# Optimization experiments

Measured on AMD Instinct MI355X. Metric: run time of the kernel, lower is better.

Reference implementation:

```python
import jax, jax.numpy as jnp
import numpy as np

B, V_IN, V_OUT, C_IN, C_OUT, SPIRAL, K_NNZ = 4, 12500, 50000, 64, 32, 9, 3

def setup_inputs() -> dict:
    key = jax.random.key(0)
    k1, k2, k3, k4, k5 = jax.random.split(key, 5)
    x = jax.random.normal(k1, (B, V_IN, C_IN), dtype=jnp.float32)
    spiral_indices = jax.random.randint(k2, (V_OUT, SPIRAL), 0, V_OUT)
    up_idx = jax.random.randint(k3, (V_OUT, K_NNZ), 0, V_IN)
    up_val = jax.random.uniform(k4, (V_OUT, K_NNZ), dtype=jnp.float32)
    weight = jax.random.normal(k5, (SPIRAL * C_IN, C_OUT), dtype=jnp.float32) / np.sqrt(SPIRAL * C_IN)
    bias = jnp.zeros((C_OUT,), dtype=jnp.float32)
    return {"x": x, "spiral_indices": spiral_indices, "up_idx": up_idx,
            "up_val": up_val, "weight": weight, "bias": bias}

def reference(x, spiral_indices, up_idx, up_val, weight, bias):
    # pool_bvc: sparse up_transform @ x, 3 nnz per output vertex
    # x: [B, V_in, C]; up_idx/up_val: [V_out, K]
    up = jnp.einsum('bvkc,vk->bvc', x[:, up_idx], up_val)  # [B, V_out, C_in]
    # SpiralConv: gather spiral neighborhoods, flatten, linear
    g = up[:, spiral_indices]                               # [B, V_out, S, C_in]
    g = g.reshape(g.shape[0], g.shape[1], -1)               # [B, V_out, S*C_in]
    y = jnp.einsum('bvf,fo->bvo', g, weight) + bias         # [B, V_out, C_out]
    return jax.nn.relu(y)
```

## Files before the change

### kernel.cpp

```cpp
#include <hip/hip_runtime.h>
#include <hip/hip_bf16.h>

#define B_     4
#define V_IN   12500
#define V_OUT  50000
#define C_IN   64
#define C_OUT  32
#define SPIRAL 9
#define K_NNZ  3
#define ROWS   (B_ * V_OUT)
#define KDIM   (SPIRAL * C_IN)
#define KSTEPS (KDIM / 32)
#define WFRAG_ELEMS (KSTEPS * 2 * 64 * 8)

#define GROUPS_PER_B (V_OUT / 16)
#define G1           2048
#define TILES_PER_B  782
#define G2           1024

typedef __attribute__((ext_vector_type(8))) short short8_t;
typedef __attribute__((ext_vector_type(4))) float floatx4;

__device__ __forceinline__ unsigned short f32_to_bf16(float f) {
    unsigned int u = __float_as_uint(f);
    unsigned int r = u + 0x7fffu + ((u >> 16) & 1u);
    return (unsigned short)(r >> 16);
}

__global__ __launch_bounds__(256) void upsample_kernel(
    const float* __restrict__ x,
    const int* __restrict__ up_idx,
    const float* __restrict__ up_val,
    const float* __restrict__ weight,
    unsigned short* __restrict__ up_bf16,
    unsigned short* __restrict__ w_frag)
{
    int tid = threadIdx.x;
    if (blockIdx.x == G1) {
        for (int idx = tid; idx < WFRAG_ELEMS; idx += 256) {
            int j     = idx & 7;
            int lane  = (idx >> 3) & 63;
            int ntile = (idx >> 9) & 1;
            int kstep = idx >> 10;
            int k = kstep * 32 + (lane >> 4) * 8 + j;
            int n = ntile * 16 + (lane & 15);
            w_frag[idx] = f32_to_bf16(weight[k * C_OUT + n]);
        }
        return;
    }
    int xcd  = blockIdx.x & 7;
    int b    = xcd >> 1;
    int h    = xcd & 1;
    int j    = blockIdx.x >> 3;
    int slot = h + 2 * j;
    int lane16 = tid & 15;
    int sub    = tid >> 4;

    const float* xb = x + (size_t)b * V_IN * C_IN;
    unsigned short* upb = up_bf16 + (size_t)b * V_OUT * C_IN;

    for (int gl = slot; gl < GROUPS_PER_B; gl += 1024) {
        int gl2  = gl + 512;
        int has2 = gl2 < GROUPS_PER_B;
        int v1 = gl * 16 + sub;
        int v2 = has2 ? gl2 * 16 + sub : v1;
        int   u10 = up_idx[v1 * K_NNZ + 0], u11 = up_idx[v1 * K_NNZ + 1], u12 = up_idx[v1 * K_NNZ + 2];
        int   u20 = up_idx[v2 * K_NNZ + 0], u21 = up_idx[v2 * K_NNZ + 1], u22 = up_idx[v2 * K_NNZ + 2];
        float c10 = up_val[v1 * K_NNZ + 0], c11 = up_val[v1 * K_NNZ + 1], c12 = up_val[v1 * K_NNZ + 2];
        float c20 = up_val[v2 * K_NNZ + 0], c21 = up_val[v2 * K_NNZ + 1], c22 = up_val[v2 * K_NNZ + 2];
        float4 xa0 = *((const float4*)(xb + (size_t)u10 * C_IN) + lane16);
        float4 xa1 = *((const float4*)(xb + (size_t)u11 * C_IN) + lane16);
        float4 xa2 = *((const float4*)(xb + (size_t)u12 * C_IN) + lane16);
        float4 xb0 = *((const float4*)(xb + (size_t)u20 * C_IN) + lane16);
        float4 xb1 = *((const float4*)(xb + (size_t)u21 * C_IN) + lane16);
        float4 xb2 = *((const float4*)(xb + (size_t)u22 * C_IN) + lane16);
        ushort4 o1, o2;
        o1.x = f32_to_bf16(c10 * xa0.x + c11 * xa1.x + c12 * xa2.x);
        o1.y = f32_to_bf16(c10 * xa0.y + c11 * xa1.y + c12 * xa2.y);
        o1.z = f32_to_bf16(c10 * xa0.z + c11 * xa1.z + c12 * xa2.z);
        o1.w = f32_to_bf16(c10 * xa0.w + c11 * xa1.w + c12 * xa2.w);
        o2.x = f32_to_bf16(c20 * xb0.x + c21 * xb1.x + c22 * xb2.x);
        o2.y = f32_to_bf16(c20 * xb0.y + c21 * xb1.y + c22 * xb2.y);
        o2.z = f32_to_bf16(c20 * xb0.z + c21 * xb1.z + c22 * xb2.z);
        o2.w = f32_to_bf16(c20 * xb0.w + c21 * xb1.w + c22 * xb2.w);
        *((ushort4*)(upb + (size_t)v1 * C_IN) + lane16) = o1;
        if (has2) *((ushort4*)(upb + (size_t)v2 * C_IN) + lane16) = o2;
    }
}

__global__ __launch_bounds__(256, 2) void gemm_kernel(
    const unsigned short* __restrict__ up_bf16,
    const int* __restrict__ spiral,
    const unsigned short* __restrict__ w_frag,
    const float* __restrict__ bias,
    float* __restrict__ out)
{
    __shared__ __align__(16) unsigned short w_lds[WFRAG_ELEMS];
    int tid = threadIdx.x;
    {
        const uint4* src = (const uint4*)w_frag;
        uint4* dst = (uint4*)w_lds;
#pragma unroll
        for (int i = 0; i < WFRAG_ELEMS / 8 / 256; i++)
            dst[tid + i * 256] = src[tid + i * 256];
    }
    __syncthreads();

    int wave = tid >> 6;
    int lane = tid & 63;
    int m    = lane & 15;
    int quad = lane >> 4;

    int xcd  = blockIdx.x & 7;
    int b    = xcd >> 1;
    int h    = xcd & 1;
    int j    = blockIdx.x >> 3;
    int slot = h + 2 * j;

    const unsigned short* upb = up_bf16 + (size_t)b * V_OUT * C_IN;
    float* outb = out + (size_t)b * V_OUT * C_OUT;

    float4 bias0 = ((const float4*)bias)[quad];
    float4 bias1 = ((const float4*)bias)[4 + quad];

    int sp[SPIRAL];
    {
        int vr = slot * 64 + wave * 16 + m;
        int v = vr < V_OUT ? vr : 0;
#pragma unroll
        for (int s = 0; s < SPIRAL; s++) sp[s] = spiral[v * SPIRAL + s];
    }

    for (int tl = slot; tl < TILES_PER_B; tl += 256) {
        short8_t g0[SPIRAL], g1[SPIRAL];
#pragma unroll
        for (int s = 0; s < SPIRAL; s++) {
            const unsigned short* rowp = upb + (size_t)sp[s] * C_IN;
            g0[s] = *(const short8_t*)(rowp + quad * 8);
            g1[s] = *(const short8_t*)(rowp + 32 + quad * 8);
        }
        int tln = tl + 256;
        if (tln < TILES_PER_B) {
            int vrn = tln * 64 + wave * 16 + m;
            int vn = vrn < V_OUT ? vrn : 0;
#pragma unroll
            for (int s = 0; s < SPIRAL; s++) sp[s] = spiral[vn * SPIRAL + s];
        }

        floatx4 acc0 = {0.f, 0.f, 0.f, 0.f};
        floatx4 acc1 = {0.f, 0.f, 0.f, 0.f};
#pragma unroll
        for (int kstep = 0; kstep < KSTEPS; kstep++) {
            short8_t gf = (kstep & 1) ? g1[kstep >> 1] : g0[kstep >> 1];
            const short8_t* wp0 = (const short8_t*)(w_lds + ((kstep * 2 + 0) * 64 + lane) * 8);
            const short8_t* wp1 = (const short8_t*)(w_lds + ((kstep * 2 + 1) * 64 + lane) * 8);
            acc0 = __builtin_amdgcn_mfma_f32_16x16x32_bf16(*wp0, gf, acc0, 0, 0, 0);
            acc1 = __builtin_amdgcn_mfma_f32_16x16x32_bf16(*wp1, gf, acc1, 0, 0, 0);
        }

        int vr = tl * 64 + wave * 16 + m;
        if (vr < V_OUT) {
            float4 o0, o1;
            o0.x = acc0[0] + bias0.x; o0.y = acc0[1] + bias0.y;
            o0.z = acc0[2] + bias0.z; o0.w = acc0[3] + bias0.w;
            o1.x = acc1[0] + bias1.x; o1.y = acc1[1] + bias1.y;
            o1.z = acc1[2] + bias1.z; o1.w = acc1[3] + bias1.w;
            o0.x = o0.x > 0.f ? o0.x : 0.f;  o0.y = o0.y > 0.f ? o0.y : 0.f;
            o0.z = o0.z > 0.f ? o0.z : 0.f;  o0.w = o0.w > 0.f ? o0.w : 0.f;
            o1.x = o1.x > 0.f ? o1.x : 0.f;  o1.y = o1.y > 0.f ? o1.y : 0.f;
            o1.z = o1.z > 0.f ? o1.z : 0.f;  o1.w = o1.w > 0.f ? o1.w : 0.f;
            float* op = outb + (size_t)vr * C_OUT;
            *(float4*)(op + quad * 4)      = o0;
            *(float4*)(op + 16 + quad * 4) = o1;
        }
    }
}

extern "C" void kernel_launch(void* const* d_in, const int* in_sizes, int n_in,
                              void* d_out, int out_size, void* d_ws, size_t ws_size,
                              hipStream_t stream) {
    const float* x      = (const float*)d_in[0];
    const int*   spiral = (const int*)d_in[1];
    const int*   up_idx = (const int*)d_in[2];
    const float* up_val = (const float*)d_in[3];
    const float* weight = (const float*)d_in[4];
    const float* bias   = (const float*)d_in[5];
    float* out = (float*)d_out;

    unsigned short* up_ws  = (unsigned short*)d_ws;
    unsigned short* w_frag = up_ws + (size_t)ROWS * C_IN;

    upsample_kernel<<<G1 + 1, 256, 0, stream>>>(x, up_idx, up_val, weight, up_ws, w_frag);
    gemm_kernel<<<G2, 256, 0, stream>>>(up_ws, spiral, w_frag, bias, out);
}
```

Measured before the change: 130.4 us.

## Split gemm gather into two passes by spiral row half, accumulate all tiles in registers

The gemm kernel now keeps accumulators for up to four tiles per wave in registers and makes two passes over the spiral neighbors. Each pass gathers only rows whose index falls in one half of the upsampled buffer, which shrinks the working set per pass to improve cache hit rates. The cost is that every row is loaded twice with masking, MFMA work doubles because zeroed fragments are still multiplied, and register pressure rises from holding several accumulators and spiral index sets.

```diff
diff --git a/kernel.cpp b/kernel.cpp
--- a/kernel.cpp
+++ b/kernel.cpp
@@ -12,11 +12,13 @@
 #define KDIM   (SPIRAL * C_IN)
 #define KSTEPS (KDIM / 32)
 #define WFRAG_ELEMS (KSTEPS * 2 * 64 * 8)
+#define HALF_V (V_OUT / 2)
 
 #define GROUPS_PER_B (V_OUT / 16)
 #define G1           2048
 #define TILES_PER_B  782
 #define G2           1024
+#define MAXT         4
 
 typedef __attribute__((ext_vector_type(8))) short short8_t;
 typedef __attribute__((ext_vector_type(4))) float floatx4;
@@ -120,59 +122,76 @@
     const unsigned short* upb = up_bf16 + (size_t)b * V_OUT * C_IN;
     float* outb = out + (size_t)b * V_OUT * C_OUT;
 
+    int ntile = 0;
+#pragma unroll
+    for (int it = 0; it < MAXT; it++)
+        if (slot + 256 * it < TILES_PER_B) ntile++;
+
+    floatx4 acc[MAXT][2];
+#pragma unroll
+    for (int it = 0; it < MAXT; it++) {
+        acc[it][0] = (floatx4){0.f, 0.f, 0.f, 0.f};
+        acc[it][1] = (floatx4){0.f, 0.f, 0.f, 0.f};
+    }
+
+    for (int pass = 0; pass < 2; pass++) {
+        int sp[MAXT][SPIRAL];
+        int valid[MAXT];
+#pragma unroll
+        for (int it = 0; it < MAXT; it++) {
+            if (it >= ntile) continue;
+            int vr = (slot + 256 * it) * 64 + wave * 16 + m;
+            valid[it] = vr < V_OUT;
+            int v = valid[it] ? vr : 0;
+#pragma unroll
+            for (int s = 0; s < SPIRAL; s++) sp[it][s] = spiral[v * SPIRAL + s];
+        }
+#pragma unroll
+        for (int s = 0; s < SPIRAL; s++) {
+            short8_t wA = *(const short8_t*)(w_lds + (((2 * s + 0) * 2 + 0) * 64 + lane) * 8);
+            short8_t wB = *(const short8_t*)(w_lds + (((2 * s + 0) * 2 + 1) * 64 + lane) * 8);
+            short8_t wC = *(const short8_t*)(w_lds + (((2 * s + 1) * 2 + 0) * 64 + lane) * 8);
+            short8_t wD = *(const short8_t*)(w_lds + (((2 * s + 1) * 2 + 1) * 64 + lane) * 8);
+#pragma unroll
+            for (int it = 0; it < MAXT; it++) {
+                if (it >= ntile) continue;
+                int inpass = (sp[it][s] < HALF_V) == (pass == 0);
+                int use = valid[it] && inpass;
+                int row = use ? sp[it][s] : 0;
+                const unsigned short* rowp = upb + (size_t)row * C_IN;
+                short8_t f0 = *(const short8_t*)(rowp + quad * 8);
+                short8_t f1 = *(const short8_t*)(rowp + 32 + quad * 8);
+                if (!use) {
+                    f0 = (short8_t){0, 0, 0, 0, 0, 0, 0, 0};
+                    f1 = (short8_t){0, 0, 0, 0, 0, 0, 0, 0};
+                }
+                acc[it][0] = __builtin_amdgcn_mfma_f32_16x16x32_bf16(wA, f0, acc[it][0], 0, 0, 0);
+                acc[it][1] = __builtin_amdgcn_mfma_f32_16x16x32_bf16(wB, f0, acc[it][1], 0, 0, 0);
+                acc[it][0] = __builtin_amdgcn_mfma_f32_16x16x32_bf16(wC, f1, acc[it][0], 0, 0, 0);
+                acc[it][1] = __builtin_amdgcn_mfma_f32_16x16x32_bf16(wD, f1, acc[it][1], 0, 0, 0);
+            }
+        }
+    }
+
     float4 bias0 = ((const float4*)bias)[quad];
     float4 bias1 = ((const float4*)bias)[4 + quad];
-
-    int sp[SPIRAL];
-    {
-        int vr = slot * 64 + wave * 16 + m;
-        int v = vr < V_OUT ? vr : 0;
-#pragma unroll
-        for (int s = 0; s < SPIRAL; s++) sp[s] = spiral[v * SPIRAL + s];
-    }
-
-    for (int tl = slot; tl < TILES_PER_B; tl += 256) {
-        short8_t g0[SPIRAL], g1[SPIRAL];
-#pragma unroll
-        for (int s = 0; s < SPIRAL; s++) {
-            const unsigned short* rowp = upb + (size_t)sp[s] * C_IN;
-            g0[s] = *(const short8_t*)(rowp + quad * 8);
-            g1[s] = *(const short8_t*)(rowp + 32 + quad * 8);
-        }
-        int tln = tl + 256;
-        if (tln < TILES_PER_B) {
-            int vrn = tln * 64 + wave * 16 + m;
-            int vn = vrn < V_OUT ? vrn : 0;
-#pragma unroll
-            for (int s = 0; s < SPIRAL; s++) sp[s] = spiral[vn * SPIRAL + s];
-        }
-
-        floatx4 acc0 = {0.f, 0.f, 0.f, 0.f};
-        floatx4 acc1 = {0.f, 0.f, 0.f, 0.f};
-#pragma unroll
-        for (int kstep = 0; kstep < KSTEPS; kstep++) {
-            short8_t gf = (kstep & 1) ? g1[kstep >> 1] : g0[kstep >> 1];
-            const short8_t* wp0 = (const short8_t*)(w_lds + ((kstep * 2 + 0) * 64 + lane) * 8);
-            const short8_t* wp1 = (const short8_t*)(w_lds + ((kstep * 2 + 1) * 64 + lane) * 8);
-            acc0 = __builtin_amdgcn_mfma_f32_16x16x32_bf16(*wp0, gf, acc0, 0, 0, 0);
-            acc1 = __builtin_amdgcn_mfma_f32_16x16x32_bf16(*wp1, gf, acc1, 0, 0, 0);
-        }
-
-        int vr = tl * 64 + wave * 16 + m;
-        if (vr < V_OUT) {
-            float4 o0, o1;
-            o0.x = acc0[0] + bias0.x; o0.y = acc0[1] + bias0.y;
-            o0.z = acc0[2] + bias0.z; o0.w = acc0[3] + bias0.w;
-            o1.x = acc1[0] + bias1.x; o1.y = acc1[1] + bias1.y;
-            o1.z = acc1[2] + bias1.z; o1.w = acc1[3] + bias1.w;
-            o0.x = o0.x > 0.f ? o0.x : 0.f;  o0.y = o0.y > 0.f ? o0.y : 0.f;
-            o0.z = o0.z > 0.f ? o0.z : 0.f;  o0.w = o0.w > 0.f ? o0.w : 0.f;
-            o1.x = o1.x > 0.f ? o1.x : 0.f;  o1.y = o1.y > 0.f ? o1.y : 0.f;
-            o1.z = o1.z > 0.f ? o1.z : 0.f;  o1.w = o1.w > 0.f ? o1.w : 0.f;
-            float* op = outb + (size_t)vr * C_OUT;
-            *(float4*)(op + quad * 4)      = o0;
-            *(float4*)(op + 16 + quad * 4) = o1;
-        }
+#pragma unroll
+    for (int it = 0; it < MAXT; it++) {
+        if (it >= ntile) continue;
+        int vr = (slot + 256 * it) * 64 + wave * 16 + m;
+        if (vr >= V_OUT) continue;
+        float4 o0, o1;
+        o0.x = acc[it][0][0] + bias0.x; o0.y = acc[it][0][1] + bias0.y;
+        o0.z = acc[it][0][2] + bias0.z; o0.w = acc[it][0][3] + bias0.w;
+        o1.x = acc[it][1][0] + bias1.x; o1.y = acc[it][1][1] + bias1.y;
+        o1.z = acc[it][1][2] + bias1.z; o1.w = acc[it][1][3] + bias1.w;
+        o0.x = o0.x > 0.f ? o0.x : 0.f;  o0.y = o0.y > 0.f ? o0.y : 0.f;
+        o0.z = o0.z > 0.f ? o0.z : 0.f;  o0.w = o0.w > 0.f ? o0.w : 0.f;
+        o1.x = o1.x > 0.f ? o1.x : 0.f;  o1.y = o1.y > 0.f ? o1.y : 0.f;
+        o1.z = o1.z > 0.f ? o1.z : 0.f;  o1.w = o1.w > 0.f ? o1.w : 0.f;
+        float* op = outb + (size_t)vr * C_OUT;
+        *(float4*)(op + quad * 4)      = o0;
+        *(float4*)(op + 16 + quad * 4) = o1;
     }
 }
 
```

After: 217.2 us. 66.6% more time.
